# Kernel optimization log

Hardware: AMD Instinct MI355X
Metric: run time of the kernel (lower is better)

## Reference

```python
import jax, jax.numpy as jnp
import numpy as np

VOCAB, D_MODEL, N_STATE, H_HEADS, LAYERS = 64, 512, 32, 16, 4
EXPAND = 2
D_INNER = EXPAND * D_MODEL          # 1024
P_HEAD = D_INNER // H_HEADS         # 64
CONV_DIM = D_INNER + 2 * N_STATE    # x, B, C share the depthwise conv
K_CONV = 4
D_IN_PROJ = 2 * D_INNER + 2 * N_STATE + H_HEADS  # z, x, B, C, dt
BATCH, SEQ = 4, 1024
EPS = 1e-5


def rmsnorm(x, w):
    return x * jax.lax.rsqrt(jnp.mean(x * x, axis=-1, keepdims=True) + EPS) * w


def silu(x):
    return x * jax.nn.sigmoid(x)


def causal_depthwise_conv(x, w, b):
    # x: [B,L,C], w: [C,K], b: [C]; causal (left) padding, depthwise groups
    xt = jnp.transpose(x, (0, 2, 1))  # [B,C,L]
    out = jax.lax.conv_general_dilated(xt, w[:, None, :], (1,), [(K_CONV - 1, 0)], feature_group_count=w.shape[0])
    return jnp.transpose(out, (0, 2, 1)) + b


def ssd(xh, dt, A, Bm, Cm, Dp):
    # Mamba2 SSD recurrence. xh [B,L,H,P], dt [B,L,H], A [H], Bm/Cm [B,L,N], Dp [H]
    dA = jnp.exp(dt * A)              # decay per (batch, step, head)
    dtx = dt[..., None] * xh          # [B,L,H,P]

    def step(h, inp):
        dA_t, dtx_t, B_t, C_t = inp
        # h: [B,H,P,N]
        h = dA_t[:, :, None, None] * h + dtx_t[..., None] * B_t[:, None, None, :]
        y = jnp.einsum('bhpn,bn->bhp', h, C_t)
        return h, y

    h0 = jnp.zeros((xh.shape[0], H_HEADS, P_HEAD, N_STATE), xh.dtype)
    _, ys = jax.lax.scan(step, h0, (jnp.moveaxis(dA, 1, 0), jnp.moveaxis(dtx, 1, 0), jnp.moveaxis(Bm, 1, 0), jnp.moveaxis(Cm, 1, 0)))
    return jnp.moveaxis(ys, 0, 1) + xh * Dp[None, None, :, None]


def mamba_block(x, norm_w, W_in, b_in, conv_w, conv_b, dt_bias, A_log, Dp, gnorm_w, W_out, b_out):
    res = x
    u = rmsnorm(x, norm_w)
    zxbcdt = u @ W_in + b_in                                # [B,L,D_IN_PROJ]
    z = zxbcdt[..., :D_INNER]
    xBC = zxbcdt[..., D_INNER:D_INNER + CONV_DIM]
    dt = zxbcdt[..., D_INNER + CONV_DIM:]                   # [B,L,H]
    xBC = silu(causal_depthwise_conv(xBC, conv_w, conv_b))
    xc = xBC[..., :D_INNER]
    Bm = xBC[..., D_INNER:D_INNER + N_STATE]
    Cm = xBC[..., D_INNER + N_STATE:]
    dt = jax.nn.softplus(dt + dt_bias)
    xh = xc.reshape(xc.shape[0], xc.shape[1], H_HEADS, P_HEAD)
    y = ssd(xh, dt, -jnp.exp(A_log), Bm, Cm, Dp)
    y = y.reshape(y.shape[0], y.shape[1], D_INNER)
    y = rmsnorm(y * silu(z), gnorm_w)                       # gated RMSNorm
    return res + y @ W_out + b_out


def forward(input_tokens, emb, norm_w, W_in, b_in, conv_w, conv_b, dt_bias, A_log, D_param, gnorm_w, W_out, b_out, head_w, head_b):
    h = emb[input_tokens]
    for i in range(LAYERS):
        h = mamba_block(h, norm_w[i], W_in[i], b_in[i], conv_w[i], conv_b[i], dt_bias[i], A_log[i], D_param[i], gnorm_w[i], W_out[i], b_out[i])
    return h @ head_w + head_b


def setup_inputs() -> dict:
    key = jax.random.key(0)
    ks = jax.random.split(key, 8)
    s = 0.02
    return {
        'input_tokens': jax.random.randint(ks[0], (BATCH, SEQ), 0, VOCAB),
        'emb': jax.random.normal(ks[1], (VOCAB, D_MODEL), jnp.float32) * s,
        'norm_w': jnp.ones((LAYERS, D_MODEL), jnp.float32),
        'W_in': jax.random.normal(ks[2], (LAYERS, D_MODEL, D_IN_PROJ), jnp.float32) * s,
        'b_in': jnp.zeros((LAYERS, D_IN_PROJ), jnp.float32),
        'conv_w': jax.random.normal(ks[3], (LAYERS, CONV_DIM, K_CONV), jnp.float32) * 0.1,
        'conv_b': jnp.zeros((LAYERS, CONV_DIM), jnp.float32),
        'dt_bias': jnp.tile(jnp.log(jnp.expm1(jnp.linspace(0.001, 0.1, H_HEADS, dtype=jnp.float32))), (LAYERS, 1)),
        'A_log': jnp.tile(jnp.log(jnp.arange(1, H_HEADS + 1, dtype=jnp.float32)), (LAYERS, 1)),
        'D_param': jnp.ones((LAYERS, H_HEADS), jnp.float32),
        'gnorm_w': jnp.ones((LAYERS, D_INNER), jnp.float32),
        'W_out': jax.random.normal(ks[4], (LAYERS, D_INNER, D_MODEL), jnp.float32) * s,
        'b_out': jnp.zeros((LAYERS, D_MODEL), jnp.float32),
        'head_w': jax.random.normal(ks[5], (D_MODEL, VOCAB), jnp.float32) * s,
        'head_b': jnp.zeros((VOCAB,), jnp.float32),
    }


def reference(input_tokens, emb, norm_w, W_in, b_in, conv_w, conv_b, dt_bias, A_log, D_param, gnorm_w, W_out, b_out, head_w, head_b):
    return forward(input_tokens, emb, norm_w, W_in, b_in, conv_w, conv_b, dt_bias, A_log, D_param, gnorm_w, W_out, b_out, head_w, head_b)
```

## Files before the change

kernel.cpp:

```cpp
#include <hip/hip_runtime.h>
#include <hip/hip_bf16.h>

#define VOCAB     64
#define D_MODEL   512
#define N_STATE   32
#define H_HEADS   16
#define LAYERS    4
#define D_INNER   1024
#define P_HEAD    64
#define CONV_DIM  1088
#define K_CONV    4
#define D_IN_PROJ 2128
#define NPAD_IN   2176
#define NPAD_HEAD 128
#define BATCH     4
#define SEQ       1024
#define NTOK      (BATCH*SEQ)
#define EPS       1e-5f
#define CL        64
#define NC        (SEQ/CL)
#define PSTR      80

typedef __bf16 bf16x8 __attribute__((ext_vector_type(8)));
typedef float  f32x4  __attribute__((ext_vector_type(4)));

__device__ __forceinline__ float sigmoidf_(float x) { return 1.f / (1.f + __expf(-x)); }
__device__ __forceinline__ float softplusf_(float x) { return (x > 20.f) ? x : log1pf(__expf(x)); }

__global__ void embed_kernel(const int* __restrict__ tok, const float* __restrict__ emb,
                             float* __restrict__ h) {
  int idx = blockIdx.x * 256 + threadIdx.x;
  if (idx >= NTOK * D_MODEL) return;
  int d = idx & (D_MODEL - 1);
  int t = idx >> 9;
  h[idx] = emb[tok[t] * D_MODEL + d];
}

__global__ void rmsnorm512_kernel(const float* __restrict__ x, const float* __restrict__ w,
                                  __bf16* __restrict__ out) {
  int tok = blockIdx.x;
  int tid = threadIdx.x;
  const float* xr = x + (size_t)tok * D_MODEL;
  float v0 = xr[tid], v1 = xr[tid + 256];
  float ss = v0 * v0 + v1 * v1;
  #pragma unroll
  for (int o = 32; o >= 1; o >>= 1) ss += __shfl_xor(ss, o);
  __shared__ float red[4];
  if ((tid & 63) == 0) red[tid >> 6] = ss;
  __syncthreads();
  float tot = red[0] + red[1] + red[2] + red[3];
  float sc = rsqrtf(tot * (1.f / D_MODEL) + EPS);
  out[(size_t)tok * D_MODEL + tid]       = (__bf16)(v0 * sc * w[tid]);
  out[(size_t)tok * D_MODEL + tid + 256] = (__bf16)(v1 * sc * w[tid + 256]);
}

__global__ void transpose_cast_kernel(const float* __restrict__ W, __bf16* __restrict__ Wt,
                                      int K, int N, int Npad) {
  W  += (size_t)blockIdx.z * K * N;
  Wt += (size_t)blockIdx.z * Npad * K;
  __shared__ float T[32][33];
  int n0 = blockIdx.x * 32, k0 = blockIdx.y * 32;
  int tx = threadIdx.x & 31, ty = threadIdx.x >> 5;
  #pragma unroll
  for (int i = 0; i < 4; i++) {
    int n = n0 + tx;
    T[ty + i * 8][tx] = (n < N) ? W[(size_t)(k0 + ty + i * 8) * N + n] : 0.f;
  }
  __syncthreads();
  #pragma unroll
  for (int i = 0; i < 4; i++)
    Wt[(size_t)(n0 + ty + i * 8) * K + k0 + tx] = (__bf16)T[tx][ty + i * 8];
}

#define TM 64
#define TN 128
#define TK 64
__global__ __launch_bounds__(256) void gemm_bf16_kernel(
    const __bf16* __restrict__ A, const __bf16* __restrict__ Bt,
    const float* __restrict__ bias, const float* __restrict__ res,
    float* __restrict__ C, __bf16* __restrict__ Cbf, int K, int N, int ldc) {
  __shared__ __bf16 As[TM * TK];
  __shared__ __bf16 Bs[TN * TK];
  int tid = threadIdx.x;
  int lane = tid & 63, wave = tid >> 6;
  int wm = wave >> 1, wn = wave & 1;
  int q = lane >> 4, l16 = lane & 15;
  size_t row0 = (size_t)blockIdx.y * TM;
  int col0 = blockIdx.x * TN;
  const __bf16* Ab = A + row0 * K;
  const __bf16* Bb = Bt + (size_t)col0 * K;

  bf16x8 pa[2], pb[4];
  #pragma unroll
  for (int r = 0; r < 2; r++) {
    int lin = r * 256 + tid;
    pa[r] = *(const bf16x8*)(Ab + (size_t)(lin >> 3) * K + (lin & 7) * 8);
  }
  #pragma unroll
  for (int r = 0; r < 4; r++) {
    int lin = r * 256 + tid;
    pb[r] = *(const bf16x8*)(Bb + (size_t)(lin >> 3) * K + (lin & 7) * 8);
  }

  f32x4 acc[2][4];
  #pragma unroll
  for (int i = 0; i < 2; i++)
    #pragma unroll
    for (int j = 0; j < 4; j++) acc[i][j] = (f32x4){0.f, 0.f, 0.f, 0.f};

  for (int k0 = 0; k0 < K; k0 += TK) {
    #pragma unroll
    for (int r = 0; r < 2; r++) { int lin = r * 256 + tid; *(bf16x8*)(As + lin * 8) = pa[r]; }
    #pragma unroll
    for (int r = 0; r < 4; r++) { int lin = r * 256 + tid; *(bf16x8*)(Bs + lin * 8) = pb[r]; }
    __syncthreads();
    int kn = k0 + TK;
    if (kn < K) {
      #pragma unroll
      for (int r = 0; r < 2; r++) {
        int lin = r * 256 + tid;
        pa[r] = *(const bf16x8*)(Ab + (size_t)(lin >> 3) * K + kn + (lin & 7) * 8);
      }
      #pragma unroll
      for (int r = 0; r < 4; r++) {
        int lin = r * 256 + tid;
        pb[r] = *(const bf16x8*)(Bb + (size_t)(lin >> 3) * K + kn + (lin & 7) * 8);
      }
    }
    #pragma unroll
    for (int ks = 0; ks < 2; ks++) {
      bf16x8 af[2], bfv[4];
      #pragma unroll
      for (int i = 0; i < 2; i++)
        af[i] = *(const bf16x8*)(As + (wm * 32 + i * 16 + l16) * TK + ks * 32 + q * 8);
      #pragma unroll
      for (int j = 0; j < 4; j++)
        bfv[j] = *(const bf16x8*)(Bs + (wn * 64 + j * 16 + l16) * TK + ks * 32 + q * 8);
      #pragma unroll
      for (int i = 0; i < 2; i++)
        #pragma unroll
        for (int j = 0; j < 4; j++)
          acc[i][j] = __builtin_amdgcn_mfma_f32_16x16x32_bf16(af[i], bfv[j], acc[i][j], 0, 0, 0);
    }
    __syncthreads();
  }

  #pragma unroll
  for (int i = 0; i < 2; i++) {
    size_t mrow = row0 + wm * 32 + i * 16 + q * 4;
    #pragma unroll
    for (int j = 0; j < 4; j++) {
      int col = col0 + wn * 64 + j * 16 + l16;
      if (col < N) {
        float bv = bias ? bias[col] : 0.f;
        #pragma unroll
        for (int rr = 0; rr < 4; rr++) {
          size_t off = (mrow + rr) * (size_t)ldc + col;
          float v = acc[i][j][rr] + bv;
          if (res) v += res[off];
          if (C)   C[off] = v;
          if (Cbf) Cbf[off] = (__bf16)v;
        }
      }
    }
  }
}


__device__ __forceinline__ void wave0_dt_cumsum(
    const __bf16* __restrict__ zxbf, const float* __restrict__ dt_bias,
    int b, int h, int t0, int tid, float* ldt, float* lcs) {
  if (tid < 64) {
    float dv = (float)zxbf[((size_t)(b * SEQ + t0 + tid)) * D_IN_PROJ + 2 * D_INNER + 2 * N_STATE + h]
               + dt_bias[h];
    float dtv = softplusf_(dv);
    float cs = dtv;
    #pragma unroll
    for (int off = 1; off < 64; off <<= 1) {
      float o = __shfl_up(cs, off);
      if (tid >= off) cs += o;
    }
    ldt[tid] = dtv;
    lcs[tid] = cs;
  }
}

__global__ __launch_bounds__(256) void ssd_local_kernel(
    const __bf16* __restrict__ zxbf, const float* __restrict__ conv_w,
    const float* __restrict__ conv_b, const float* __restrict__ dt_bias,
    const float* __restrict__ A_log,
    float* __restrict__ Slocal, float* __restrict__ dAprod) {
  int blk = blockIdx.x;
  int c = blk % NC;
  int h = (blk / NC) % H_HEADS;
  int b = blk / (NC * H_HEADS);
  int tid = threadIdx.x;
  int lane = tid & 63, wave = tid >> 6;
  int q = lane >> 4, l16 = lane & 15;
  int t0 = c * CL;
  float A = -__expf(A_log[h]);
  __shared__ __bf16 rawx[68][64];
  __shared__ __bf16 rawB[68][32];
  __shared__ __bf16 lxT[64][PSTR];
  __shared__ __bf16 lBT[32][PSTR];
  __shared__ float ldt[64], lcs[64];
  for (int i = tid; i < 68 * 8; i += 256) {
    int r = i >> 3, c0 = (i & 7) * 8;
    int gr = t0 - 3 + r;
    bf16x8 v;
    #pragma unroll
    for (int k = 0; k < 8; k++) v[k] = (__bf16)0.f;
    if (gr >= 0)
      v = *(const bf16x8*)(zxbf + ((size_t)(b * SEQ + gr)) * D_IN_PROJ + D_INNER + h * 64 + c0);
    *(bf16x8*)(&rawx[r][c0]) = v;
  }
  for (int i = tid; i < 68 * 4; i += 256) {
    int r = i >> 2, c0 = (i & 3) * 8;
    int gr = t0 - 3 + r;
    bf16x8 v;
    #pragma unroll
    for (int k = 0; k < 8; k++) v[k] = (__bf16)0.f;
    if (gr >= 0)
      v = *(const bf16x8*)(zxbf + ((size_t)(b * SEQ + gr)) * D_IN_PROJ + 2 * D_INNER + c0);
    *(bf16x8*)(&rawB[r][c0]) = v;
  }
  wave0_dt_cumsum(zxbf, dt_bias, b, h, t0, tid, ldt, lcs);
  __syncthreads();
  float cs63 = lcs[63];
  {
    int p = tid & 63;
    const float* w = conv_w + (h * 64 + p) * K_CONV;
    float w0 = w[0], w1 = w[1], w2 = w[2], w3 = w[3];
    float cb = conv_b[h * 64 + p];
    for (int i = tid; i < CL * 64; i += 256) {
      int t = i >> 6;
      float a = cb + w0 * (float)rawx[t][p] + w1 * (float)rawx[t + 1][p]
                   + w2 * (float)rawx[t + 2][p] + w3 * (float)rawx[t + 3][p];
      lxT[p][t] = (__bf16)(a * sigmoidf_(a));
    }
  }
  {
    int n = tid & 31;
    const float* w = conv_w + (D_INNER + n) * K_CONV;
    float w0 = w[0], w1 = w[1], w2 = w[2], w3 = w[3];
    float cb = conv_b[D_INNER + n];
    for (int i = tid; i < CL * 32; i += 256) {
      int t = i >> 5;
      float a = cb + w0 * (float)rawB[t][n] + w1 * (float)rawB[t + 1][n]
                   + w2 * (float)rawB[t + 2][n] + w3 * (float)rawB[t + 3][n];
      float v = a * sigmoidf_(a);
      float wt = ldt[t] * __expf(A * (cs63 - lcs[t]));
      lBT[n][t] = (__bf16)(v * wt);
    }
  }
  __syncthreads();
  f32x4 acc[2];
  acc[0] = (f32x4){0.f,0.f,0.f,0.f}; acc[1] = (f32x4){0.f,0.f,0.f,0.f};
  #pragma unroll
  for (int kb = 0; kb < 2; kb++) {
    bf16x8 af = *(const bf16x8*)(&lxT[wave * 16 + l16][kb * 32 + q * 8]);
    #pragma unroll
    for (int j = 0; j < 2; j++) {
      bf16x8 bf = *(const bf16x8*)(&lBT[l16 + 16 * j][kb * 32 + q * 8]);
      acc[j] = __builtin_amdgcn_mfma_f32_16x16x32_bf16(af, bf, acc[j], 0, 0, 0);
    }
  }
  float* dst = Slocal + (size_t)blk * 2048;
  #pragma unroll
  for (int j = 0; j < 2; j++) {
    int n = l16 + 16 * j;
    #pragma unroll
    for (int rr = 0; rr < 4; rr++) {
      int p = wave * 16 + q * 4 + rr;
      dst[p * 32 + n] = acc[j][rr];
    }
  }
  if (tid == 0) dAprod[blk] = __expf(A * cs63);
}

__global__ void ssd_combine_kernel(float* __restrict__ S, const float* __restrict__ dAprod) {
  int bh = blockIdx.x;
  int e = threadIdx.x * 8;
  float st[8] = {};
  for (int c = 0; c < NC; c++) {
    float* ptr = S + ((size_t)(bh * NC + c)) * 2048 + e;
    float pr = dAprod[bh * NC + c];
    float tmp[8];
    #pragma unroll
    for (int j = 0; j < 8; j++) tmp[j] = ptr[j];
    #pragma unroll
    for (int j = 0; j < 8; j++) { ptr[j] = st[j]; st[j] = pr * st[j] + tmp[j]; }
  }
}

__global__ __launch_bounds__(256) void ssd_out_kernel(
    const __bf16* __restrict__ zxbf, const float* __restrict__ conv_w,
    const float* __restrict__ conv_b, const float* __restrict__ dt_bias,
    const float* __restrict__ A_log, const float* __restrict__ Dp,
    const float* __restrict__ Sstart, float* __restrict__ y) {
  int blk = blockIdx.x;
  int c = blk % NC;
  int h = (blk / NC) % H_HEADS;
  int b = blk / (NC * H_HEADS);
  int tid = threadIdx.x;
  int lane = tid & 63, wave = tid >> 6;
  int q = lane >> 4, l16 = lane & 15;
  int t0 = c * CL;
  float A = -__expf(A_log[h]);
  float D = Dp[h];
  __shared__ __bf16 rawbuf[2 * 68 * 64];
  __shared__ __bf16 lxT[64][PSTR];
  __shared__ __bf16 lB[64][32];
  __shared__ __bf16 lC[64][32];
  __shared__ __bf16 lS[64][32];
  __shared__ float ldt[64], lcs[64];
  __bf16* rawx = rawbuf;
  __bf16* rawBC = rawbuf + 68 * 64;
  for (int i = tid; i < 68 * 8; i += 256) {
    int r = i >> 3, c0 = (i & 7) * 8;
    int gr = t0 - 3 + r;
    bf16x8 vx, vbc;
    #pragma unroll
    for (int k = 0; k < 8; k++) { vx[k] = (__bf16)0.f; vbc[k] = (__bf16)0.f; }
    if (gr >= 0) {
      const __bf16* rowp = zxbf + ((size_t)(b * SEQ + gr)) * D_IN_PROJ;
      vx  = *(const bf16x8*)(rowp + D_INNER + h * 64 + c0);
      vbc = *(const bf16x8*)(rowp + 2 * D_INNER + c0);
    }
    *(bf16x8*)(rawx + r * 64 + c0)  = vx;
    *(bf16x8*)(rawBC + r * 64 + c0) = vbc;
  }
  wave0_dt_cumsum(zxbf, dt_bias, b, h, t0, tid, ldt, lcs);
  __syncthreads();
  {
    int p = tid & 63;
    const float* w = conv_w + (h * 64 + p) * K_CONV;
    float w0 = w[0], w1 = w[1], w2 = w[2], w3 = w[3];
    float cb = conv_b[h * 64 + p];
    for (int i = tid; i < CL * 64; i += 256) {
      int t = i >> 6;
      float a = cb + w0 * (float)rawx[t * 64 + p] + w1 * (float)rawx[(t + 1) * 64 + p]
                   + w2 * (float)rawx[(t + 2) * 64 + p] + w3 * (float)rawx[(t + 3) * 64 + p];
      lxT[p][t] = (__bf16)(a * sigmoidf_(a));
    }
  }
  {
    int col = tid & 63;
    const float* w = conv_w + (D_INNER + col) * K_CONV;
    float w0 = w[0], w1 = w[1], w2 = w[2], w3 = w[3];
    float cb = conv_b[D_INNER + col];
    for (int i = tid; i < CL * 64; i += 256) {
      int t = i >> 6;
      float a = cb + w0 * (float)rawBC[t * 64 + col] + w1 * (float)rawBC[(t + 1) * 64 + col]
                   + w2 * (float)rawBC[(t + 2) * 64 + col] + w3 * (float)rawBC[(t + 3) * 64 + col];
      float v = a * sigmoidf_(a);
      if (col < 32) lB[t][col] = (__bf16)v; else lC[t][col - 32] = (__bf16)v;
    }
  }
  {
    const float* src = Sstart + (size_t)blk * 2048;
    for (int i = tid; i < 2048; i += 256) lS[i >> 5][i & 31] = (__bf16)src[i];
  }
  __syncthreads();
  bf16x8 afC = *(const bf16x8*)(&lC[wave * 16 + l16][q * 8]);
  f32x4 accG[4], accI[4], accY[4];
  #pragma unroll
  for (int j = 0; j < 4; j++) {
    accG[j] = (f32x4){0.f,0.f,0.f,0.f};
    accI[j] = (f32x4){0.f,0.f,0.f,0.f};
    accY[j] = (f32x4){0.f,0.f,0.f,0.f};
  }
  #pragma unroll
  for (int j = 0; j < 4; j++) {
    bf16x8 bf = *(const bf16x8*)(&lB[l16 + 16 * j][q * 8]);
    accG[j] = __builtin_amdgcn_mfma_f32_16x16x32_bf16(afC, bf, accG[j], 0, 0, 0);
  }
  #pragma unroll
  for (int j = 0; j < 4; j++) {
    bf16x8 bf = *(const bf16x8*)(&lS[l16 + 16 * j][q * 8]);
    accI[j] = __builtin_amdgcn_mfma_f32_16x16x32_bf16(afC, bf, accI[j], 0, 0, 0);
  }
  __bf16* pP = rawbuf + wave * 16 * PSTR;
  #pragma unroll
  for (int j = 0; j < 4; j++) {
    int s = l16 + 16 * j;
    float css = lcs[s], dts = ldt[s];
    #pragma unroll
    for (int rr = 0; rr < 4; rr++) {
      int tl = q * 4 + rr;
      int t = wave * 16 + tl;
      float val = accG[j][rr] * __expf(A * (lcs[t] - css)) * dts;
      if (s == t) val += D;
      if (s > t) val = 0.f;
      pP[tl * PSTR + s] = (__bf16)val;
    }
  }
  #pragma unroll
  for (int kb = 0; kb < 2; kb++) {
    bf16x8 afP = *(const bf16x8*)(pP + l16 * PSTR + kb * 32 + q * 8);
    #pragma unroll
    for (int j = 0; j < 4; j++) {
      bf16x8 bf = *(const bf16x8*)(&lxT[l16 + 16 * j][kb * 32 + q * 8]);
      accY[j] = __builtin_amdgcn_mfma_f32_16x16x32_bf16(afP, bf, accY[j], 0, 0, 0);
    }
  }
  #pragma unroll
  for (int rr = 0; rr < 4; rr++) {
    int t = wave * 16 + q * 4 + rr;
    float cumt = __expf(A * lcs[t]);
    float* yrow = y + ((size_t)(b * SEQ + t0 + t)) * D_INNER + h * 64;
    #pragma unroll
    for (int j = 0; j < 4; j++) {
      int p = l16 + 16 * j;
      yrow[p] = accY[j][rr] + cumt * accI[j][rr];
    }
  }
}

__global__ void gate_norm_kernel(const __bf16* __restrict__ zxbf, const float* __restrict__ gw,
                                 const float* __restrict__ y, __bf16* __restrict__ ybf) {
  int tok = blockIdx.x;
  int tid = threadIdx.x;
  const __bf16* zr = zxbf + (size_t)tok * D_IN_PROJ;
  const float* yr = y + (size_t)tok * D_INNER;
  float v[4];
  float ss = 0.f;
  #pragma unroll
  for (int i = 0; i < 4; i++) {
    int d = tid + i * 256;
    float z = (float)zr[d];
    float g = yr[d] * z * sigmoidf_(z);
    v[i] = g;
    ss += g * g;
  }
  #pragma unroll
  for (int o = 32; o >= 1; o >>= 1) ss += __shfl_xor(ss, o);
  __shared__ float red[4];
  if ((tid & 63) == 0) red[tid >> 6] = ss;
  __syncthreads();
  float tot = red[0] + red[1] + red[2] + red[3];
  float sc = rsqrtf(tot * (1.f / D_INNER) + EPS);
  #pragma unroll
  for (int i = 0; i < 4; i++) {
    int d = tid + i * 256;
    ybf[(size_t)tok * D_INNER + d] = (__bf16)(v[i] * sc * gw[d]);
  }
}

extern "C" void kernel_launch(void* const* d_in, const int* in_sizes, int n_in,
                              void* d_out, int out_size, void* d_ws, size_t ws_size,
                              hipStream_t stream) {
  const int*   tok     = (const int*)  d_in[0];
  const float* emb     = (const float*)d_in[1];
  const float* norm_w  = (const float*)d_in[2];
  const float* W_in    = (const float*)d_in[3];
  const float* b_in    = (const float*)d_in[4];
  const float* conv_w  = (const float*)d_in[5];
  const float* conv_b  = (const float*)d_in[6];
  const float* dt_bias = (const float*)d_in[7];
  const float* A_log   = (const float*)d_in[8];
  const float* D_par   = (const float*)d_in[9];
  const float* gnorm_w = (const float*)d_in[10];
  const float* W_out   = (const float*)d_in[11];
  const float* b_out   = (const float*)d_in[12];
  const float* head_w  = (const float*)d_in[13];
  const float* head_b  = (const float*)d_in[14];
  float* out = (float*)d_out;

  char* p = (char*)d_ws;
  auto alloc = [&](size_t bytes) { void* r = (void*)p; p += (bytes + 255) & ~(size_t)255; return r; };
  float*  h      = (float*) alloc((size_t)NTOK * D_MODEL * 4);
  float*  y      = (float*) alloc((size_t)NTOK * D_INNER * 4);
  float*  slocal = (float*) alloc((size_t)BATCH * H_HEADS * NC * P_HEAD * N_STATE * 4);
  float*  daprod = (float*) alloc((size_t)BATCH * H_HEADS * NC * 4);
  __bf16* zxbf   = (__bf16*)alloc((size_t)NTOK * D_IN_PROJ * 2);
  __bf16* ubf    = (__bf16*)alloc((size_t)NTOK * D_MODEL * 2);
  __bf16* ybf    = (__bf16*)alloc((size_t)NTOK * D_INNER * 2);
  __bf16* hbf    = (__bf16*)alloc((size_t)NTOK * D_MODEL * 2);
  __bf16* WtIn   = (__bf16*)alloc((size_t)LAYERS * NPAD_IN * D_MODEL * 2);
  __bf16* WtOut  = (__bf16*)alloc((size_t)LAYERS * D_MODEL * D_INNER * 2);
  __bf16* WtHead = (__bf16*)alloc((size_t)NPAD_HEAD * D_MODEL * 2);

  transpose_cast_kernel<<<dim3(NPAD_IN / 32, D_MODEL / 32, LAYERS), 256, 0, stream>>>(
      W_in, WtIn, D_MODEL, D_IN_PROJ, NPAD_IN);
  transpose_cast_kernel<<<dim3(D_MODEL / 32, D_INNER / 32, LAYERS), 256, 0, stream>>>(
      W_out, WtOut, D_INNER, D_MODEL, D_MODEL);
  transpose_cast_kernel<<<dim3(NPAD_HEAD / 32, D_MODEL / 32, 1), 256, 0, stream>>>(
      head_w, WtHead, D_MODEL, VOCAB, NPAD_HEAD);

  embed_kernel<<<(NTOK * D_MODEL + 255) / 256, 256, 0, stream>>>(tok, emb, h);

  for (int l = 0; l < LAYERS; l++) {
    rmsnorm512_kernel<<<NTOK, 256, 0, stream>>>(h, norm_w + (size_t)l * D_MODEL, ubf);

    gemm_bf16_kernel<<<dim3(NPAD_IN / TN, NTOK / TM), 256, 0, stream>>>(
        ubf, WtIn + (size_t)l * NPAD_IN * D_MODEL, b_in + (size_t)l * D_IN_PROJ,
        nullptr, nullptr, zxbf, D_MODEL, D_IN_PROJ, D_IN_PROJ);

    ssd_local_kernel<<<BATCH * H_HEADS * NC, 256, 0, stream>>>(
        zxbf, conv_w + (size_t)l * CONV_DIM * K_CONV, conv_b + (size_t)l * CONV_DIM,
        dt_bias + (size_t)l * H_HEADS, A_log + (size_t)l * H_HEADS, slocal, daprod);
    ssd_combine_kernel<<<BATCH * H_HEADS, 256, 0, stream>>>(slocal, daprod);
    ssd_out_kernel<<<BATCH * H_HEADS * NC, 256, 0, stream>>>(
        zxbf, conv_w + (size_t)l * CONV_DIM * K_CONV, conv_b + (size_t)l * CONV_DIM,
        dt_bias + (size_t)l * H_HEADS, A_log + (size_t)l * H_HEADS,
        D_par + (size_t)l * H_HEADS, slocal, y);

    gate_norm_kernel<<<NTOK, 256, 0, stream>>>(zxbf, gnorm_w + (size_t)l * D_INNER, y, ybf);

    gemm_bf16_kernel<<<dim3(D_MODEL / TN, NTOK / TM), 256, 0, stream>>>(
        ybf, WtOut + (size_t)l * D_MODEL * D_INNER, b_out + (size_t)l * D_MODEL, h, h,
        (l == LAYERS - 1) ? hbf : nullptr, D_INNER, D_MODEL, D_MODEL);
  }

  gemm_bf16_kernel<<<dim3(NPAD_HEAD / TN, NTOK / TM), 256, 0, stream>>>(
      hbf, WtHead, head_b, nullptr, out, nullptr, D_MODEL, VOCAB, VOCAB);
}
```

Measured before the change: 502.0 us.

## Fuse RMSNorm into input GEMM and gated norm into output GEMM

Removes the standalone rmsnorm and gate_norm kernels. The input projection GEMM now reads fp32 hidden state, computes per-row RMS scale in a prologue, and normalizes/casts on the fly when staging A tiles. The output GEMM computes the gated (silu(z)*y) RMSNorm scale in a prologue and applies the gate/norm while staging, using a narrower N tile (64) to increase block count. This saves launches and intermediate bf16 round trips but every column block redundantly recomputes row norms and reads fp32 A (more A bandwidth per tile).

```diff
diff --git a/kernel.cpp b/kernel.cpp
--- a/kernel.cpp
+++ b/kernel.cpp
@@ -36,24 +36,6 @@
   h[idx] = emb[tok[t] * D_MODEL + d];
 }
 
-__global__ void rmsnorm512_kernel(const float* __restrict__ x, const float* __restrict__ w,
-                                  __bf16* __restrict__ out) {
-  int tok = blockIdx.x;
-  int tid = threadIdx.x;
-  const float* xr = x + (size_t)tok * D_MODEL;
-  float v0 = xr[tid], v1 = xr[tid + 256];
-  float ss = v0 * v0 + v1 * v1;
-  #pragma unroll
-  for (int o = 32; o >= 1; o >>= 1) ss += __shfl_xor(ss, o);
-  __shared__ float red[4];
-  if ((tid & 63) == 0) red[tid >> 6] = ss;
-  __syncthreads();
-  float tot = red[0] + red[1] + red[2] + red[3];
-  float sc = rsqrtf(tot * (1.f / D_MODEL) + EPS);
-  out[(size_t)tok * D_MODEL + tid]       = (__bf16)(v0 * sc * w[tid]);
-  out[(size_t)tok * D_MODEL + tid + 256] = (__bf16)(v1 * sc * w[tid + 256]);
-}
-
 __global__ void transpose_cast_kernel(const float* __restrict__ W, __bf16* __restrict__ Wt,
                                       int K, int N, int Npad) {
   W  += (size_t)blockIdx.z * K * N;
@@ -75,10 +57,279 @@
 #define TM 64
 #define TN 128
 #define TK 64
+__global__ __launch_bounds__(256) void gemm_in_fused(
+    const float* __restrict__ Hsrc, const float* __restrict__ nw,
+    const __bf16* __restrict__ Bt, const float* __restrict__ bias,
+    __bf16* __restrict__ Cbf) {
+  __shared__ __bf16 As[TM * TK];
+  __shared__ __bf16 Bs[TN * TK];
+  __shared__ float lnw[D_MODEL];
+  __shared__ float red[64][4];
+  __shared__ float sc[64];
+  int tid = threadIdx.x;
+  int lane = tid & 63, wave = tid >> 6;
+  int wm = wave >> 1, wn = wave & 1;
+  int q = lane >> 4, l16 = lane & 15;
+  size_t row0 = (size_t)blockIdx.y * TM;
+  int col0 = blockIdx.x * TN;
+  const float* Ab = Hsrc + row0 * D_MODEL;
+  const __bf16* Bb = Bt + (size_t)col0 * D_MODEL;
+
+  bf16x8 pb[4];
+  f32x4 pa[2][2];
+  #pragma unroll
+  for (int r = 0; r < 4; r++) {
+    int lin = r * 256 + tid;
+    pb[r] = *(const bf16x8*)(Bb + (size_t)(lin >> 3) * D_MODEL + (lin & 7) * 8);
+  }
+  #pragma unroll
+  for (int r = 0; r < 2; r++) {
+    int lin = r * 256 + tid;
+    const float* ap = Ab + (size_t)(lin >> 3) * D_MODEL + (lin & 7) * 8;
+    pa[r][0] = *(const f32x4*)(ap);
+    pa[r][1] = *(const f32x4*)(ap + 4);
+  }
+  for (int i = tid; i < D_MODEL; i += 256) lnw[i] = nw[i];
+  {
+    int r = tid >> 2, gq = tid & 3;
+    const float* hp = Ab + (size_t)r * D_MODEL + gq * 128;
+    float ss = 0.f;
+    #pragma unroll
+    for (int i = 0; i < 32; i++) {
+      f32x4 v = *(const f32x4*)(hp + i * 4);
+      ss += v[0]*v[0] + v[1]*v[1] + v[2]*v[2] + v[3]*v[3];
+    }
+    red[r][gq] = ss;
+  }
+  __syncthreads();
+  if (tid < 64)
+    sc[tid] = rsqrtf((red[tid][0] + red[tid][1] + red[tid][2] + red[tid][3]) * (1.f / D_MODEL) + EPS);
+  __syncthreads();
+
+  f32x4 acc[2][4];
+  #pragma unroll
+  for (int i = 0; i < 2; i++)
+    #pragma unroll
+    for (int j = 0; j < 4; j++) acc[i][j] = (f32x4){0.f, 0.f, 0.f, 0.f};
+
+  for (int k0 = 0; k0 < D_MODEL; k0 += TK) {
+    #pragma unroll
+    for (int r = 0; r < 2; r++) {
+      int lin = r * 256 + tid;
+      int row = lin >> 3, kc = (lin & 7) * 8;
+      float s = sc[row];
+      bf16x8 o;
+      #pragma unroll
+      for (int j = 0; j < 4; j++) o[j] = (__bf16)(pa[r][0][j] * s * lnw[k0 + kc + j]);
+      #pragma unroll
+      for (int j = 0; j < 4; j++) o[4 + j] = (__bf16)(pa[r][1][j] * s * lnw[k0 + kc + 4 + j]);
+      *(bf16x8*)(As + lin * 8) = o;
+    }
+    #pragma unroll
+    for (int r = 0; r < 4; r++) { int lin = r * 256 + tid; *(bf16x8*)(Bs + lin * 8) = pb[r]; }
+    __syncthreads();
+    int kn = k0 + TK;
+    if (kn < D_MODEL) {
+      #pragma unroll
+      for (int r = 0; r < 2; r++) {
+        int lin = r * 256 + tid;
+        const float* ap = Ab + (size_t)(lin >> 3) * D_MODEL + kn + (lin & 7) * 8;
+        pa[r][0] = *(const f32x4*)(ap);
+        pa[r][1] = *(const f32x4*)(ap + 4);
+      }
+      #pragma unroll
+      for (int r = 0; r < 4; r++) {
+        int lin = r * 256 + tid;
+        pb[r] = *(const bf16x8*)(Bb + (size_t)(lin >> 3) * D_MODEL + kn + (lin & 7) * 8);
+      }
+    }
+    #pragma unroll
+    for (int ks = 0; ks < 2; ks++) {
+      bf16x8 af[2], bfv[4];
+      #pragma unroll
+      for (int i = 0; i < 2; i++)
+        af[i] = *(const bf16x8*)(As + (wm * 32 + i * 16 + l16) * TK + ks * 32 + q * 8);
+      #pragma unroll
+      for (int j = 0; j < 4; j++)
+        bfv[j] = *(const bf16x8*)(Bs + (wn * 64 + j * 16 + l16) * TK + ks * 32 + q * 8);
+      #pragma unroll
+      for (int i = 0; i < 2; i++)
+        #pragma unroll
+        for (int j = 0; j < 4; j++)
+          acc[i][j] = __builtin_amdgcn_mfma_f32_16x16x32_bf16(af[i], bfv[j], acc[i][j], 0, 0, 0);
+    }
+    __syncthreads();
+  }
+
+  #pragma unroll
+  for (int i = 0; i < 2; i++) {
+    size_t mrow = row0 + wm * 32 + i * 16 + q * 4;
+    #pragma unroll
+    for (int j = 0; j < 4; j++) {
+      int col = col0 + wn * 64 + j * 16 + l16;
+      if (col < D_IN_PROJ) {
+        float bv = bias[col];
+        #pragma unroll
+        for (int rr = 0; rr < 4; rr++) {
+          size_t off = (mrow + rr) * (size_t)D_IN_PROJ + col;
+          Cbf[off] = (__bf16)(acc[i][j][rr] + bv);
+        }
+      }
+    }
+  }
+}
+
+#define OTN 64
+__global__ __launch_bounds__(256) void gemm_out_fused(
+    const float* __restrict__ Ysrc, const __bf16* __restrict__ zxbf,
+    const float* __restrict__ gw, const __bf16* __restrict__ Bt,
+    const float* __restrict__ bias, float* __restrict__ Hres,
+    __bf16* __restrict__ Cbf) {
+  __shared__ __bf16 As[TM * TK];
+  __shared__ __bf16 Bs[OTN * TK];
+  __shared__ float lgw[D_INNER];
+  __shared__ float red[64][4];
+  __shared__ float sc[64];
+  int tid = threadIdx.x;
+  int lane = tid & 63, wave = tid >> 6;
+  int wm = wave >> 1, wn = wave & 1;
+  int q = lane >> 4, l16 = lane & 15;
+  size_t row0 = (size_t)blockIdx.y * TM;
+  int col0 = blockIdx.x * OTN;
+  const float* Ay = Ysrc + row0 * D_INNER;
+  const __bf16* Az = zxbf + row0 * D_IN_PROJ;
+  const __bf16* Bb = Bt + (size_t)col0 * D_INNER;
+
+  bf16x8 pb[2];
+  f32x4 pay[2][2];
+  bf16x8 paz[2];
+  #pragma unroll
+  for (int r = 0; r < 2; r++) {
+    int lin = r * 256 + tid;
+    pb[r] = *(const bf16x8*)(Bb + (size_t)(lin >> 3) * D_INNER + (lin & 7) * 8);
+  }
+  #pragma unroll
+  for (int r = 0; r < 2; r++) {
+    int lin = r * 256 + tid;
+    int row = lin >> 3, kc = (lin & 7) * 8;
+    const float* yp = Ay + (size_t)row * D_INNER + kc;
+    pay[r][0] = *(const f32x4*)(yp);
+    pay[r][1] = *(const f32x4*)(yp + 4);
+    paz[r]    = *(const bf16x8*)(Az + (size_t)row * D_IN_PROJ + kc);
+  }
+  for (int i = tid; i < D_INNER; i += 256) lgw[i] = gw[i];
+  {
+    int r = tid >> 2, gq = tid & 3;
+    const float* yp = Ay + (size_t)r * D_INNER + gq * 256;
+    const __bf16* zp = Az + (size_t)r * D_IN_PROJ + gq * 256;
+    float ss = 0.f;
+    #pragma unroll
+    for (int i = 0; i < 32; i++) {
+      f32x4 v0 = *(const f32x4*)(yp + i * 8);
+      f32x4 v1 = *(const f32x4*)(yp + i * 8 + 4);
+      bf16x8 vz = *(const bf16x8*)(zp + i * 8);
+      #pragma unroll
+      for (int j = 0; j < 4; j++) {
+        float z0 = (float)vz[j];
+        float g0 = v0[j] * z0 * sigmoidf_(z0);
+        float z1 = (float)vz[4 + j];
+        float g1 = v1[j] * z1 * sigmoidf_(z1);
+        ss += g0 * g0 + g1 * g1;
+      }
+    }
+    red[r][gq] = ss;
+  }
+  __syncthreads();
+  if (tid < 64)
+    sc[tid] = rsqrtf((red[tid][0] + red[tid][1] + red[tid][2] + red[tid][3]) * (1.f / D_INNER) + EPS);
+  __syncthreads();
+
+  f32x4 acc[2][2];
+  #pragma unroll
+  for (int i = 0; i < 2; i++)
+    #pragma unroll
+    for (int j = 0; j < 2; j++) acc[i][j] = (f32x4){0.f, 0.f, 0.f, 0.f};
+
+  for (int k0 = 0; k0 < D_INNER; k0 += TK) {
+    #pragma unroll
+    for (int r = 0; r < 2; r++) {
+      int lin = r * 256 + tid;
+      int row = lin >> 3, kc = (lin & 7) * 8;
+      float s = sc[row];
+      bf16x8 o;
+      #pragma unroll
+      for (int j = 0; j < 4; j++) {
+        float zz = (float)paz[r][j];
+        float g = pay[r][0][j] * zz * sigmoidf_(zz);
+        o[j] = (__bf16)(g * s * lgw[k0 + kc + j]);
+      }
+      #pragma unroll
+      for (int j = 0; j < 4; j++) {
+        float zz = (float)paz[r][4 + j];
+        float g = pay[r][1][j] * zz * sigmoidf_(zz);
+        o[4 + j] = (__bf16)(g * s * lgw[k0 + kc + 4 + j]);
+      }
+      *(bf16x8*)(As + lin * 8) = o;
+    }
+    #pragma unroll
+    for (int r = 0; r < 2; r++) { int lin = r * 256 + tid; *(bf16x8*)(Bs + lin * 8) = pb[r]; }
+    __syncthreads();
+    int kn = k0 + TK;
+    if (kn < D_INNER) {
+      #pragma unroll
+      for (int r = 0; r < 2; r++) {
+        int lin = r * 256 + tid;
+        int row = lin >> 3, kc = (lin & 7) * 8;
+        const float* yp = Ay + (size_t)row * D_INNER + kn + kc;
+        pay[r][0] = *(const f32x4*)(yp);
+        pay[r][1] = *(const f32x4*)(yp + 4);
+        paz[r]    = *(const bf16x8*)(Az + (size_t)row * D_IN_PROJ + kn + kc);
+      }
+      #pragma unroll
+      for (int r = 0; r < 2; r++) {
+        int lin = r * 256 + tid;
+        pb[r] = *(const bf16x8*)(Bb + (size_t)(lin >> 3) * D_INNER + kn + (lin & 7) * 8);
+      }
+    }
+    #pragma unroll
+    for (int ks = 0; ks < 2; ks++) {
+      bf16x8 af[2], bfv[2];
+      #pragma unroll
+      for (int i = 0; i < 2; i++)
+        af[i] = *(const bf16x8*)(As + (wm * 32 + i * 16 + l16) * TK + ks * 32 + q * 8);
+      #pragma unroll
+      for (int j = 0; j < 2; j++)
+        bfv[j] = *(const bf16x8*)(Bs + (wn * 32 + j * 16 + l16) * TK + ks * 32 + q * 8);
+      #pragma unroll
+      for (int i = 0; i < 2; i++)
+        #pragma unroll
+        for (int j = 0; j < 2; j++)
+          acc[i][j] = __builtin_amdgcn_mfma_f32_16x16x32_bf16(af[i], bfv[j], acc[i][j], 0, 0, 0);
+    }
+    __syncthreads();
+  }
+
+  #pragma unroll
+  for (int i = 0; i < 2; i++) {
+    size_t mrow = row0 + wm * 32 + i * 16 + q * 4;
+    #pragma unroll
+    for (int j = 0; j < 2; j++) {
+      int col = col0 + wn * 32 + j * 16 + l16;
+      float bv = bias[col];
+      #pragma unroll
+      for (int rr = 0; rr < 4; rr++) {
+        size_t off = (mrow + rr) * (size_t)D_MODEL + col;
+        float v = acc[i][j][rr] + bv + Hres[off];
+        Hres[off] = v;
+        if (Cbf) Cbf[off] = (__bf16)v;
+      }
+    }
+  }
+}
+
 __global__ __launch_bounds__(256) void gemm_bf16_kernel(
     const __bf16* __restrict__ A, const __bf16* __restrict__ Bt,
-    const float* __restrict__ bias, const float* __restrict__ res,
-    float* __restrict__ C, __bf16* __restrict__ Cbf, int K, int N, int ldc) {
+    const float* __restrict__ bias, float* __restrict__ C, int K, int N, int ldc) {
   __shared__ __bf16 As[TM * TK];
   __shared__ __bf16 Bs[TN * TK];
   int tid = threadIdx.x;
@@ -101,7 +352,6 @@
     int lin = r * 256 + tid;
     pb[r] = *(const bf16x8*)(Bb + (size_t)(lin >> 3) * K + (lin & 7) * 8);
   }
-
   f32x4 acc[2][4];
   #pragma unroll
   for (int i = 0; i < 2; i++)
@@ -144,7 +394,6 @@
     }
     __syncthreads();
   }
-
   #pragma unroll
   for (int i = 0; i < 2; i++) {
     size_t mrow = row0 + wm * 32 + i * 16 + q * 4;
@@ -152,20 +401,14 @@
     for (int j = 0; j < 4; j++) {
       int col = col0 + wn * 64 + j * 16 + l16;
       if (col < N) {
-        float bv = bias ? bias[col] : 0.f;
+        float bv = bias[col];
         #pragma unroll
-        for (int rr = 0; rr < 4; rr++) {
-          size_t off = (mrow + rr) * (size_t)ldc + col;
-          float v = acc[i][j][rr] + bv;
-          if (res) v += res[off];
-          if (C)   C[off] = v;
-          if (Cbf) Cbf[off] = (__bf16)v;
-        }
-      }
-    }
-  }
-}
-
+        for (int rr = 0; rr < 4; rr++)
+          C[(mrow + rr) * (size_t)ldc + col] = acc[i][j][rr] + bv;
+      }
+    }
+  }
+}
 
 __device__ __forceinline__ void wave0_dt_cumsum(
     const __bf16* __restrict__ zxbf, const float* __restrict__ dt_bias,
@@ -417,36 +660,6 @@
   }
 }
 
-__global__ void gate_norm_kernel(const __bf16* __restrict__ zxbf, const float* __restrict__ gw,
-                                 const float* __restrict__ y, __bf16* __restrict__ ybf) {
-  int tok = blockIdx.x;
-  int tid = threadIdx.x;
-  const __bf16* zr = zxbf + (size_t)tok * D_IN_PROJ;
-  const float* yr = y + (size_t)tok * D_INNER;
-  float v[4];
-  float ss = 0.f;
-  #pragma unroll
-  for (int i = 0; i < 4; i++) {
-    int d = tid + i * 256;
-    float z = (float)zr[d];
-    float g = yr[d] * z * sigmoidf_(z);
-    v[i] = g;
-    ss += g * g;
-  }
-  #pragma unroll
-  for (int o = 32; o >= 1; o >>= 1) ss += __shfl_xor(ss, o);
-  __shared__ float red[4];
-  if ((tid & 63) == 0) red[tid >> 6] = ss;
-  __syncthreads();
-  float tot = red[0] + red[1] + red[2] + red[3];
-  float sc = rsqrtf(tot * (1.f / D_INNER) + EPS);
-  #pragma unroll
-  for (int i = 0; i < 4; i++) {
-    int d = tid + i * 256;
-    ybf[(size_t)tok * D_INNER + d] = (__bf16)(v[i] * sc * gw[d]);
-  }
-}
-
 extern "C" void kernel_launch(void* const* d_in, const int* in_sizes, int n_in,
                               void* d_out, int out_size, void* d_ws, size_t ws_size,
                               hipStream_t stream) {
@@ -474,8 +687,6 @@
   float*  slocal = (float*) alloc((size_t)BATCH * H_HEADS * NC * P_HEAD * N_STATE * 4);
   float*  daprod = (float*) alloc((size_t)BATCH * H_HEADS * NC * 4);
   __bf16* zxbf   = (__bf16*)alloc((size_t)NTOK * D_IN_PROJ * 2);
-  __bf16* ubf    = (__bf16*)alloc((size_t)NTOK * D_MODEL * 2);
-  __bf16* ybf    = (__bf16*)alloc((size_t)NTOK * D_INNER * 2);
   __bf16* hbf    = (__bf16*)alloc((size_t)NTOK * D_MODEL * 2);
   __bf16* WtIn   = (__bf16*)alloc((size_t)LAYERS * NPAD_IN * D_MODEL * 2);
   __bf16* WtOut  = (__bf16*)alloc((size_t)LAYERS * D_MODEL * D_INNER * 2);
@@ -491,11 +702,9 @@
   embed_kernel<<<(NTOK * D_MODEL + 255) / 256, 256, 0, stream>>>(tok, emb, h);
 
   for (int l = 0; l < LAYERS; l++) {
-    rmsnorm512_kernel<<<NTOK, 256, 0, stream>>>(h, norm_w + (size_t)l * D_MODEL, ubf);
-
-    gemm_bf16_kernel<<<dim3(NPAD_IN / TN, NTOK / TM), 256, 0, stream>>>(
-        ubf, WtIn + (size_t)l * NPAD_IN * D_MODEL, b_in + (size_t)l * D_IN_PROJ,
-        nullptr, nullptr, zxbf, D_MODEL, D_IN_PROJ, D_IN_PROJ);
+    gemm_in_fused<<<dim3(NPAD_IN / TN, NTOK / TM), 256, 0, stream>>>(
+        h, norm_w + (size_t)l * D_MODEL,
+        WtIn + (size_t)l * NPAD_IN * D_MODEL, b_in + (size_t)l * D_IN_PROJ, zxbf);
 
     ssd_local_kernel<<<BATCH * H_HEADS * NC, 256, 0, stream>>>(
         zxbf, conv_w + (size_t)l * CONV_DIM * K_CONV, conv_b + (size_t)l * CONV_DIM,
@@ -506,13 +715,12 @@
         dt_bias + (size_t)l * H_HEADS, A_log + (size_t)l * H_HEADS,
         D_par + (size_t)l * H_HEADS, slocal, y);
 
-    gate_norm_kernel<<<NTOK, 256, 0, stream>>>(zxbf, gnorm_w + (size_t)l * D_INNER, y, ybf);
-
-    gemm_bf16_kernel<<<dim3(D_MODEL / TN, NTOK / TM), 256, 0, stream>>>(
-        ybf, WtOut + (size_t)l * D_MODEL * D_INNER, b_out + (size_t)l * D_MODEL, h, h,
-        (l == LAYERS - 1) ? hbf : nullptr, D_INNER, D_MODEL, D_MODEL);
+    gemm_out_fused<<<dim3(D_MODEL / OTN, NTOK / TM), 256, 0, stream>>>(
+        y, zxbf, gnorm_w + (size_t)l * D_INNER,
+        WtOut + (size_t)l * D_MODEL * D_INNER, b_out + (size_t)l * D_MODEL, h,
+        (l == LAYERS - 1) ? hbf : nullptr);
   }
 
   gemm_bf16_kernel<<<dim3(NPAD_HEAD / TN, NTOK / TM), 256, 0, stream>>>(
-      hbf, WtHead, head_b, nullptr, out, nullptr, D_MODEL, VOCAB, VOCAB);
-}
+      hbf, WtHead, head_b, out, D_MODEL, VOCAB, VOCAB);
+}
```

Result: slower. 872.7 us (+73.9%).
